# Performance work log

Measured on AMD Instinct MI355X. Metric: run time of the kernel, lower is better.

Reference implementation:

```python
import jax, jax.numpy as jnp
import numpy as np

# geomloss SamplesLoss('sinkhorn', p=2, blur=0.05, scaling=0.5, debias=True) math
P = 2
BLUR = 0.05
SCALING = 0.5
DIAMETER = 64.0  # static conservative bound on point-cloud diameter for randn D=64 data


def _eps_schedule():
    eps_list = []
    e = DIAMETER ** P
    target = BLUR ** P
    while e > target:
        eps_list.append(e)
        e *= SCALING ** P
    eps_list.append(target)
    return np.array(eps_list, dtype=np.float32)


def _cost(x, y):
    # C_ij = ||x_i - y_j||^2 / 2   (p=2 cost of geomloss)
    sq = (jnp.sum(x * x, -1)[:, :, None] * 0.5
          + jnp.sum(y * y, -1)[:, None, :] * 0.5
          - jnp.einsum('bnd,bmd->bnm', x, y))
    return jnp.maximum(sq, 0.0)


def _softmin(eps, C, h):
    # f_i = -eps * log sum_j exp(h_j - C_ij / eps);  C: (B,N,M), h: (B,M)
    return -eps * jax.nn.logsumexp(h[:, None, :] - C / eps, axis=-1)


def setup_inputs() -> dict:
    key = jax.random.key(0)
    k1, k2, k3, k4 = jax.random.split(key, 4)
    B, N, M, D = 8, 2048, 2048, 64
    x = jax.random.normal(k1, (B, N, D), dtype=jnp.float32)
    y = jax.random.normal(k2, (B, M, D), dtype=jnp.float32)
    w1 = jax.random.uniform(k3, (B, N), dtype=jnp.float32) + 0.01
    w2 = jax.random.uniform(k4, (B, M), dtype=jnp.float32) + 0.01
    w1 = w1 / jnp.sum(w1, axis=-1, keepdims=True)
    w2 = w2 / jnp.sum(w2, axis=-1, keepdims=True)
    return {'x': x, 'y': y, 'w1': w1, 'w2': w2}


def _sinkhorn_divergence(x, y, w1, w2):
    a_log = jnp.log(w1)
    b_log = jnp.log(w2)
    eps_list = jnp.asarray(_eps_schedule())

    # --- Sinkhorn loop on detached quantities (geomloss detaches the loop) ---
    xd = jax.lax.stop_gradient(x)
    yd = jax.lax.stop_gradient(y)
    ald = jax.lax.stop_gradient(a_log)
    bld = jax.lax.stop_gradient(b_log)
    C_xy_d = _cost(xd, yd)
    C_yx_d = jnp.swapaxes(C_xy_d, 1, 2)
    C_xx_d = _cost(xd, xd)
    C_yy_d = _cost(yd, yd)

    eps0 = eps_list[0]
    f_ab = _softmin(eps0, C_xy_d, bld)
    g_ba = _softmin(eps0, C_yx_d, ald)
    f_aa = _softmin(eps0, C_xx_d, ald)
    g_bb = _softmin(eps0, C_yy_d, bld)

    def step(carry, eps):
        f_ab, g_ba, f_aa, g_bb = carry
        ft = _softmin(eps, C_xy_d, bld + g_ba / eps)
        gt = _softmin(eps, C_yx_d, ald + f_ab / eps)
        f_aa_t = _softmin(eps, C_xx_d, ald + f_aa / eps)
        g_bb_t = _softmin(eps, C_yy_d, bld + g_bb / eps)
        return (0.5 * (f_ab + ft), 0.5 * (g_ba + gt),
                0.5 * (f_aa + f_aa_t), 0.5 * (g_bb + g_bb_t)), None

    (f_ab, g_ba, f_aa, g_bb), _ = jax.lax.scan(step, (f_ab, g_ba, f_aa, g_bb), eps_list)

    # --- last extrapolation at eps = blur^p, differentiable ---
    eps = eps_list[-1]
    C_xy = _cost(x, y)
    C_yx = jnp.swapaxes(C_xy, 1, 2)
    C_xx = _cost(x, x)
    C_yy = _cost(y, y)
    f_ab_f = _softmin(eps, C_xy, b_log + g_ba / eps)
    g_ba_f = _softmin(eps, C_yx, a_log + f_ab / eps)
    f_aa_f = _softmin(eps, C_xx, a_log + f_aa / eps)
    g_bb_f = _softmin(eps, C_yy, b_log + g_bb / eps)

    # debiased sinkhorn cost per batch element
    loss = (jnp.sum(w1 * (f_ab_f - f_aa_f), axis=-1)
            + jnp.sum(w2 * (g_ba_f - g_bb_f), axis=-1))
    return loss


def reference(x, y, w1, w2):
    loss = _sinkhorn_divergence(x, y, w1, w2)
    return jnp.mean(loss)  # reduction='mean'
```

## Files before the change

kernel.cpp:

```cpp
#include <hip/hip_runtime.h>

#define NB 8
#define NN 2048
#define MM 2048
#define DD 64
#define NMAT ((size_t)NN * (size_t)MM)
#define NCHK 16
#define TS 128

#define CSCALE 320.0f
#define CDEC   (1.0f / CSCALE)
#define LOG2E  1.4426950408889634f
#define LN2    0.6931471805599453f

typedef _Float16 half_t;
typedef __attribute__((ext_vector_type(8))) _Float16 f16x8;
typedef __attribute__((ext_vector_type(4))) float f32x4;

__device__ unsigned short g_C[3 * NB * NMAT];
__device__ half_t g_xh[NB * NN * DD];
__device__ half_t g_yh[NB * MM * DD];
__device__ float g_fab[3][NB * NN], g_gba[3][NB * NN];
__device__ float g_faa[3][NB * NN], g_gbb[3][NB * NN];
__device__ float g_alog[NB * NN], g_blog[NB * NN];
__device__ float g_xn[NB * NN], g_yn[NB * NN];
__device__ float g_h0[NB * MM], g_h1[NB * NN], g_h2[NB * NN], g_h3[NB * MM];
__device__ float2 g_pfab[NB * NCHK * NN];
__device__ float2 g_pgba[NB * NCHK * NN];
__device__ float2 g_pfaa[NB * NCHK * NN];
__device__ float2 g_pgbb[NB * NCHK * NN];

__global__ __launch_bounds__(256) void prep_kernel(
    const float* __restrict__ x, const float* __restrict__ y,
    const float* __restrict__ w1, const float* __restrict__ w2)
{
  int gid = blockIdx.x * 256 + threadIdx.x;
  if (gid < NB * NN) {
    g_alog[gid] = logf(w1[gid]);
    g_blog[gid] = logf(w2[gid]);
  }
  int lane = threadIdx.x & 63;
  int row = blockIdx.x * 4 + (threadIdx.x >> 6);
  float xv = x[(size_t)row * DD + lane];
  float yv = y[(size_t)row * DD + lane];
  g_xh[(size_t)row * DD + lane] = (half_t)xv;
  g_yh[(size_t)row * DD + lane] = (half_t)yv;
  float sx = xv * xv;
  float sy = yv * yv;
#pragma unroll
  for (int off = 32; off > 0; off >>= 1) {
    sx += __shfl_down(sx, off);
    sy += __shfl_down(sy, off);
  }
  if (lane == 0) {
    g_xn[row] = 0.5f * sx;
    g_yn[row] = 0.5f * sy;
  }
}

__global__ __launch_bounds__(256) void cost_mfma()
{
  const int slab = blockIdx.z >> 3;
  const int b = blockIdx.z & 7;
  int I, J;
  if (slab) {
    if (blockIdx.x >= 136) return;
    int rem = blockIdx.x, ii = 0;
    while (rem >= NCHK - ii) { rem -= NCHK - ii; ++ii; }
    I = ii; J = ii + rem;
  } else {
    I = blockIdx.x >> 4;
    J = blockIdx.x & 15;
  }

  const half_t* Ah = (slab == 2) ? g_yh : g_xh;
  const half_t* Bh = (slab == 0) ? g_yh : ((slab == 1) ? g_xh : g_yh);
  const float* na = (slab == 2) ? g_yn : g_xn;
  const float* nbp = (slab == 0) ? g_yn : ((slab == 1) ? g_xn : g_yn);
  unsigned short* Cout = g_C + (size_t)slab * NB * NMAT + (size_t)b * NMAT;

  const int t = threadIdx.x;
  const int w = t >> 6, lane = t & 63;
  const int m = lane & 15, quad = lane >> 4;
  const int i0 = I * TS, j0 = J * TS;

  const half_t* Abase = Ah + ((size_t)b * NN + i0 + 32 * w + m) * DD + quad * 8;
  const half_t* Bbase = Bh + ((size_t)b * MM + j0 + m) * DD + quad * 8;

  f32x4 acc[2][8];
#pragma unroll
  for (int g = 0; g < 2; ++g)
#pragma unroll
    for (int c = 0; c < 8; ++c) acc[g][c] = (f32x4){0.f, 0.f, 0.f, 0.f};

#pragma unroll
  for (int s = 0; s < 2; ++s) {
    f16x8 a0 = *(const f16x8*)(Abase + s * 32);
    f16x8 a1 = *(const f16x8*)(Abase + (size_t)16 * DD + s * 32);
#pragma unroll
    for (int c = 0; c < 8; ++c) {
      f16x8 bf = *(const f16x8*)(Bbase + (size_t)(16 * c) * DD + s * 32);
      acc[0][c] = __builtin_amdgcn_mfma_f32_16x16x32_f16(a0, bf, acc[0][c], 0, 0, 0);
      acc[1][c] = __builtin_amdgcn_mfma_f32_16x16x32_f16(a1, bf, acc[1][c], 0, 0, 0);
    }
  }

  __shared__ unsigned short tile[TS * TS];
  float4 xr[2];
#pragma unroll
  for (int g = 0; g < 2; ++g)
    xr[g] = *(const float4*)(na + b * NN + i0 + 32 * w + 16 * g + 4 * quad);
#pragma unroll
  for (int c = 0; c < 8; ++c) {
    float yv = nbp[b * MM + j0 + 16 * c + m];
#pragma unroll
    for (int g = 0; g < 2; ++g) {
      float xg[4] = {xr[g].x, xr[g].y, xr[g].z, xr[g].w};
#pragma unroll
      for (int r = 0; r < 4; ++r) {
        float cv = fmaxf(xg[r] + yv - acc[g][c][r], 0.f);
        unsigned int u = __float2uint_rn(fminf(cv * CSCALE, 65535.f));
        tile[(32 * w + 16 * g + 4 * quad + r) * TS + 16 * c + m] = (unsigned short)u;
      }
    }
  }
  __syncthreads();

  const uint4* tl = (const uint4*)tile;
#pragma unroll
  for (int p = 0; p < 8; ++p) {
    int u = p * 256 + t;
    int row = u >> 4, c8 = (u & 15) * 8;
    *(uint4*)(Cout + (size_t)(i0 + row) * MM + j0 + c8) = tl[u];
  }
}

__global__ __launch_bounds__(256) void hprep_kernel(
    const float* __restrict__ fab_in, const float* __restrict__ gba_in,
    const float* __restrict__ faa_in, const float* __restrict__ gbb_in,
    float gs)
{
  int i = blockIdx.x * 256 + threadIdx.x;
  g_h0[i] = fmaf(gs, gba_in[i], g_blog[i]);
  g_h1[i] = fmaf(gs, fab_in[i], g_alog[i]);
  g_h2[i] = fmaf(gs, faa_in[i], g_alog[i]);
  g_h3[i] = fmaf(gs, gbb_in[i], g_blog[i]);
}

struct TileArgs {
  const unsigned short* C;
  const float* hrow;
  const float* hcol;
  float2* prow;
  float2* pcol;
  int sym;
};

__global__ __launch_bounds__(256) void tile_pass(
    TileArgs T0, TileArgs T1, TileArgs T2, float inv_eps)
{
  TileArgs A = (blockIdx.z == 0) ? T0 : (blockIdx.z == 1) ? T1 : T2;
  int I, J;
  if (A.sym) {
    if (blockIdx.x >= 136) return;
    int rem = blockIdx.x, ii = 0;
    while (rem >= NCHK - ii) { rem -= NCHK - ii; ++ii; }
    I = ii; J = ii + rem;
  } else {
    I = blockIdx.x >> 4;
    J = blockIdx.x & 15;
  }
  const int b = blockIdx.y;
  const int t = threadIdx.x;
  const int ctr = t & 15;
  const int rtr = t >> 4;
  const float cs2 = -inv_eps * CDEC * LOG2E;

  const unsigned short* Cb = A.C + (size_t)b * NMAT
                           + (size_t)(I * TS) * MM + J * TS;

  float hr2[8], hc2[8];
  {
    const float* hrp = A.hrow + (size_t)b * MM + J * TS + ctr * 8;
    const float* hcp = A.hcol + (size_t)b * MM + I * TS + rtr * 8;
#pragma unroll
    for (int k = 0; k < 8; ++k) {
      hr2[k] = hrp[k] * LOG2E;
      hc2[k] = hcp[k] * LOG2E;
    }
  }

  uint4 cu[8];
#pragma unroll
  for (int r8 = 0; r8 < 8; ++r8)
    cu[r8] = *(const uint4*)(Cb + (size_t)(rtr * 8 + r8) * MM + ctr * 8);

  __shared__ float redC[TS][17];
  __shared__ float colM[TS];

  float rm[8], cm[8];
#pragma unroll
  for (int k = 0; k < 8; ++k) { rm[k] = -3.0e38f; cm[k] = -3.0e38f; }
#pragma unroll
  for (int r8 = 0; r8 < 8; ++r8) {
    float u[8];
    u[0] = (float)(cu[r8].x & 0xffff);
    u[1] = (float)(cu[r8].x >> 16);
    u[2] = (float)(cu[r8].y & 0xffff);
    u[3] = (float)(cu[r8].y >> 16);
    u[4] = (float)(cu[r8].z & 0xffff);
    u[5] = (float)(cu[r8].z >> 16);
    u[6] = (float)(cu[r8].w & 0xffff);
    u[7] = (float)(cu[r8].w >> 16);
#pragma unroll
    for (int c8 = 0; c8 < 8; ++c8) {
      rm[r8] = fmaxf(rm[r8], fmaf(u[c8], cs2, hr2[c8]));
      cm[c8] = fmaxf(cm[c8], fmaf(u[c8], cs2, hc2[r8]));
    }
  }
#pragma unroll
  for (int mask = 1; mask < 16; mask <<= 1)
#pragma unroll
    for (int k = 0; k < 8; ++k)
      rm[k] = fmaxf(rm[k], __shfl_xor(rm[k], mask));
#pragma unroll
  for (int c8 = 0; c8 < 8; ++c8) redC[ctr * 8 + c8][rtr] = cm[c8];
  __syncthreads();
  if (t < TS) {
    float m = redC[t][0];
#pragma unroll
    for (int k = 1; k < 16; ++k) m = fmaxf(m, redC[t][k]);
    colM[t] = m;
  }
  __syncthreads();
  float cmv[8];
#pragma unroll
  for (int c8 = 0; c8 < 8; ++c8) cmv[c8] = colM[ctr * 8 + c8];

  float rs[8], cs[8];
#pragma unroll
  for (int k = 0; k < 8; ++k) { rs[k] = 0.f; cs[k] = 0.f; }
#pragma unroll
  for (int r8 = 0; r8 < 8; ++r8) {
    float u[8];
    u[0] = (float)(cu[r8].x & 0xffff);
    u[1] = (float)(cu[r8].x >> 16);
    u[2] = (float)(cu[r8].y & 0xffff);
    u[3] = (float)(cu[r8].y >> 16);
    u[4] = (float)(cu[r8].z & 0xffff);
    u[5] = (float)(cu[r8].z >> 16);
    u[6] = (float)(cu[r8].w & 0xffff);
    u[7] = (float)(cu[r8].w >> 16);
#pragma unroll
    for (int c8 = 0; c8 < 8; ++c8) {
      rs[r8] += __builtin_amdgcn_exp2f(fmaf(u[c8], cs2, hr2[c8]) - rm[r8]);
      cs[c8] += __builtin_amdgcn_exp2f(fmaf(u[c8], cs2, hc2[r8]) - cmv[c8]);
    }
  }
#pragma unroll
  for (int mask = 1; mask < 16; mask <<= 1)
#pragma unroll
    for (int k = 0; k < 8; ++k)
      rs[k] += __shfl_xor(rs[k], mask);
  if (ctr < 8) {
    A.prow[((size_t)b * NCHK + J) * NN + I * TS + rtr * 8 + ctr]
        = make_float2(rm[ctr], rs[ctr]);
  }
  __syncthreads();
#pragma unroll
  for (int c8 = 0; c8 < 8; ++c8) redC[ctr * 8 + c8][rtr] = cs[c8];
  __syncthreads();
  if (t < TS && !(A.sym && I == J)) {
    float s = 0.f;
#pragma unroll
    for (int k = 0; k < 16; ++k) s += redC[t][k];
    A.pcol[((size_t)b * NCHK + I) * NN + J * TS + t] = make_float2(colM[t], s);
  }
}

struct MergeArgs {
  const float2* part;
  const float* fold;
  float* fout;
  const float* hbase;
  float* hout;
};

__global__ __launch_bounds__(256) void merge4(
    MergeArgs M0, MergeArgs M1, MergeArgs M2, MergeArgs M3,
    float eps, float alpha, float beta, float nextgs)
{
  MergeArgs A = (blockIdx.z == 0) ? M0 : (blockIdx.z == 1) ? M1
              : (blockIdx.z == 2) ? M2 : M3;
  const int b = blockIdx.y;
  const int i = blockIdx.x * 256 + threadIdx.x;
  float2 p[NCHK];
#pragma unroll
  for (int k = 0; k < NCHK; ++k)
    p[k] = A.part[((size_t)b * NCHK + k) * NN + i];
  float M = p[0].x;
#pragma unroll
  for (int k = 1; k < NCHK; ++k) M = fmaxf(M, p[k].x);
  float S = 0.f;
#pragma unroll
  for (int k = 0; k < NCHK; ++k)
    S += p[k].y * __builtin_amdgcn_exp2f(p[k].x - M);
  float ft = -eps * LN2 * (M + __builtin_amdgcn_logf(S));
  int idx = b * NN + i;
  float fnew = alpha * A.fold[idx] + beta * ft;
  A.fout[idx] = fnew;
  A.hout[idx] = fmaf(nextgs, fnew, A.hbase[idx]);
}

__global__ __launch_bounds__(256) void loss_kernel(
    const float* __restrict__ w1, const float* __restrict__ w2,
    float* __restrict__ out)
{
  __shared__ float red[256];
  float acc = 0.f;
  for (int idx = threadIdx.x; idx < NB * NN; idx += 256) {
    acc += w1[idx] * (g_fab[2][idx] - g_faa[2][idx])
         + w2[idx] * (g_gba[2][idx] - g_gbb[2][idx]);
  }
  red[threadIdx.x] = acc;
  __syncthreads();
  for (int s = 128; s > 0; s >>= 1) {
    if (threadIdx.x < s) red[threadIdx.x] += red[threadIdx.x + s];
    __syncthreads();
  }
  if (threadIdx.x == 0) out[0] = red[0] * (1.0f / NB);
}

extern "C" void kernel_launch(void* const* d_in, const int* in_sizes, int n_in,
                              void* d_out, int out_size, void* d_ws, size_t ws_size,
                              hipStream_t stream)
{
  const float* x = (const float*)d_in[0];
  const float* y = (const float*)d_in[1];
  const float* w1 = (const float*)d_in[2];
  const float* w2 = (const float*)d_in[3];
  float* out = (float*)d_out;

  unsigned short* Cbase;
  hipGetSymbolAddress((void**)&Cbase, HIP_SYMBOL(g_C));
  unsigned short* Cxy = Cbase + 0ull * NB * NMAT;
  unsigned short* Cxx = Cbase + 1ull * NB * NMAT;
  unsigned short* Cyy = Cbase + 2ull * NB * NMAT;
  float *h0, *h1, *h2, *h3, *fabp, *gbap, *faap, *gbbp, *alog, *blog;
  float2 *pfab, *pgba, *pfaa, *pgbb;
  hipGetSymbolAddress((void**)&h0, HIP_SYMBOL(g_h0));
  hipGetSymbolAddress((void**)&h1, HIP_SYMBOL(g_h1));
  hipGetSymbolAddress((void**)&h2, HIP_SYMBOL(g_h2));
  hipGetSymbolAddress((void**)&h3, HIP_SYMBOL(g_h3));
  hipGetSymbolAddress((void**)&fabp, HIP_SYMBOL(g_fab));
  hipGetSymbolAddress((void**)&gbap, HIP_SYMBOL(g_gba));
  hipGetSymbolAddress((void**)&faap, HIP_SYMBOL(g_faa));
  hipGetSymbolAddress((void**)&gbbp, HIP_SYMBOL(g_gbb));
  hipGetSymbolAddress((void**)&alog, HIP_SYMBOL(g_alog));
  hipGetSymbolAddress((void**)&blog, HIP_SYMBOL(g_blog));
  hipGetSymbolAddress((void**)&pfab, HIP_SYMBOL(g_pfab));
  hipGetSymbolAddress((void**)&pgba, HIP_SYMBOL(g_pgba));
  hipGetSymbolAddress((void**)&pfaa, HIP_SYMBOL(g_pfaa));
  hipGetSymbolAddress((void**)&pgbb, HIP_SYMBOL(g_pgbb));

  auto fab = [&](int s) { return fabp + (size_t)s * NB * NN; };
  auto gba = [&](int s) { return gbap + (size_t)s * NB * NN; };
  auto faa = [&](int s) { return faap + (size_t)s * NB * NN; };
  auto gbb = [&](int s) { return gbbp + (size_t)s * NB * NN; };

  float eps_list[32];
  int ne = 0;
  {
    double v = 64.0 * 64.0;
    double tgt = 0.05 * 0.05;
    while (v > tgt) { eps_list[ne++] = (float)v; v *= 0.25; }
    eps_list[ne++] = (float)tgt;
  }

  prep_kernel<<<4096, 256, 0, stream>>>(x, y, w1, w2);

  cost_mfma<<<dim3(256, 1, 24), 256, 0, stream>>>();

  dim3 tg(256, NB, 3);
  dim3 mg(NN / 256, NB, 4);

  auto launch_iter = [&](float eps, float alpha, float beta, float nextgs,
                         int in, int outsel) {
    float inv = 1.0f / eps;
    TileArgs T0 = {Cxy, h0, h1, pfab, pgba, 0};
    TileArgs T1 = {Cxx, h2, h2, pfaa, pfaa, 1};
    TileArgs T2 = {Cyy, h3, h3, pgbb, pgbb, 1};
    tile_pass<<<tg, 256, 0, stream>>>(T0, T1, T2, inv);
    MergeArgs M0 = {pfab, fab(in), fab(outsel), alog, h1};
    MergeArgs M1 = {pgba, gba(in), gba(outsel), blog, h0};
    MergeArgs M2 = {pfaa, faa(in), faa(outsel), alog, h2};
    MergeArgs M3 = {pgbb, gbb(in), gbb(outsel), blog, h3};
    merge4<<<mg, 256, 0, stream>>>(M0, M1, M2, M3, eps, alpha, beta, nextgs);
  };

  hprep_kernel<<<64, 256, 0, stream>>>(fab(0), gba(0), faa(0), gbb(0), 0.f);
  launch_iter(eps_list[0], 0.f, 1.f, 1.0f / eps_list[0], 0, 0);

  int cur = 0;
  for (int k = 0; k < ne; ++k) {
    int nxt = 1 - cur;
    float nextgs = 1.0f / ((k < ne - 1) ? eps_list[k + 1] : eps_list[ne - 1]);
    launch_iter(eps_list[k], 0.5f, 0.5f, nextgs, cur, nxt);
    cur = nxt;
  }

  launch_iter(eps_list[ne - 1], 0.f, 1.f, 0.f, cur, 2);

  loss_kernel<<<1, 256, 0, stream>>>(w1, w2, out);
}
```

Baseline: 717.5 us.

## Store cost tiles in MFMA fragment order and compact the tile grid

The quantized cost matrices are now stored tile-contiguously in the MFMA accumulator fragment layout. The cost kernel can therefore write each thread's packed values directly, without the LDS transpose and its barrier. The tile pass reads each tile with fully contiguous uint4 loads and does its column reductions with cross-lane shuffles, which shrinks the shared-memory reduction from 16 partials per column to 4. The grid is also compacted to 528 live tiles per batch (256 + 136 + 136) instead of launching 768 blocks and exiting the unused symmetric ones. The costs are extra shuffle work and more complex index mapping on the write-out of row results.

```diff
diff --git a/kernel.cpp b/kernel.cpp
--- a/kernel.cpp
+++ b/kernel.cpp
@@ -7,6 +7,8 @@
 #define NMAT ((size_t)NN * (size_t)MM)
 #define NCHK 16
 #define TS 128
+#define NTILE 528
+#define TELEM 16384
 
 #define CSCALE 320.0f
 #define CDEC   (1.0f / CSCALE)
@@ -17,7 +19,7 @@
 typedef __attribute__((ext_vector_type(8))) _Float16 f16x8;
 typedef __attribute__((ext_vector_type(4))) float f32x4;
 
-__device__ unsigned short g_C[3 * NB * NMAT];
+__device__ unsigned short g_C[(size_t)NB * NTILE * TELEM];
 __device__ half_t g_xh[NB * NN * DD];
 __device__ half_t g_yh[NB * MM * DD];
 __device__ float g_fab[3][NB * NN], g_gba[3][NB * NN];
@@ -30,6 +32,17 @@
 __device__ float2 g_pfaa[NB * NCHK * NN];
 __device__ float2 g_pgbb[NB * NCHK * NN];
 
+__device__ __forceinline__ void tile_decode(int xid, int& slab, int& I, int& J)
+{
+  int tid;
+  if (xid < 256)      { slab = 0; tid = xid; I = tid >> 4; J = tid & 15; return; }
+  else if (xid < 392) { slab = 1; tid = xid - 256; }
+  else                { slab = 2; tid = xid - 392; }
+  int rem = tid, ii = 0;
+  while (rem >= NCHK - ii) { rem -= NCHK - ii; ++ii; }
+  I = ii; J = ii + rem;
+}
+
 __global__ __launch_bounds__(256) void prep_kernel(
     const float* __restrict__ x, const float* __restrict__ y,
     const float* __restrict__ w1, const float* __restrict__ w2)
@@ -60,24 +73,14 @@
 
 __global__ __launch_bounds__(256) void cost_mfma()
 {
-  const int slab = blockIdx.z >> 3;
-  const int b = blockIdx.z & 7;
-  int I, J;
-  if (slab) {
-    if (blockIdx.x >= 136) return;
-    int rem = blockIdx.x, ii = 0;
-    while (rem >= NCHK - ii) { rem -= NCHK - ii; ++ii; }
-    I = ii; J = ii + rem;
-  } else {
-    I = blockIdx.x >> 4;
-    J = blockIdx.x & 15;
-  }
+  int slab, I, J;
+  tile_decode(blockIdx.x, slab, I, J);
+  const int b = blockIdx.y;
 
   const half_t* Ah = (slab == 2) ? g_yh : g_xh;
   const half_t* Bh = (slab == 0) ? g_yh : ((slab == 1) ? g_xh : g_yh);
   const float* na = (slab == 2) ? g_yn : g_xn;
   const float* nbp = (slab == 0) ? g_yn : ((slab == 1) ? g_xn : g_yn);
-  unsigned short* Cout = g_C + (size_t)slab * NB * NMAT + (size_t)b * NMAT;
 
   const int t = threadIdx.x;
   const int w = t >> 6, lane = t & 63;
@@ -105,33 +108,31 @@
     }
   }
 
-  __shared__ unsigned short tile[TS * TS];
   float4 xr[2];
 #pragma unroll
   for (int g = 0; g < 2; ++g)
     xr[g] = *(const float4*)(na + b * NN + i0 + 32 * w + 16 * g + 4 * quad);
-#pragma unroll
-  for (int c = 0; c < 8; ++c) {
-    float yv = nbp[b * MM + j0 + 16 * c + m];
-#pragma unroll
-    for (int g = 0; g < 2; ++g) {
-      float xg[4] = {xr[g].x, xr[g].y, xr[g].z, xr[g].w};
-#pragma unroll
-      for (int r = 0; r < 4; ++r) {
-        float cv = fmaxf(xg[r] + yv - acc[g][c][r], 0.f);
-        unsigned int u = __float2uint_rn(fminf(cv * CSCALE, 65535.f));
-        tile[(32 * w + 16 * g + 4 * quad + r) * TS + 16 * c + m] = (unsigned short)u;
-      }
+  float yv[8];
+#pragma unroll
+  for (int c = 0; c < 8; ++c) yv[c] = nbp[b * MM + j0 + 16 * c + m];
+
+  uint4* Cout = (uint4*)(g_C + ((size_t)b * NTILE + blockIdx.x) * TELEM);
+#pragma unroll
+  for (int k = 0; k < 8; ++k) {
+    int g = k >> 2, r = k & 3;
+    float xg = (r == 0) ? xr[g].x : (r == 1) ? xr[g].y : (r == 2) ? xr[g].z : xr[g].w;
+    unsigned int u[8];
+#pragma unroll
+    for (int c = 0; c < 8; ++c) {
+      float cv = fmaxf(xg + yv[c] - acc[g][c][r], 0.f);
+      u[c] = __float2uint_rn(fminf(cv * CSCALE, 65535.f));
     }
-  }
-  __syncthreads();
-
-  const uint4* tl = (const uint4*)tile;
-#pragma unroll
-  for (int p = 0; p < 8; ++p) {
-    int u = p * 256 + t;
-    int row = u >> 4, c8 = (u & 15) * 8;
-    *(uint4*)(Cout + (size_t)(i0 + row) * MM + j0 + c8) = tl[u];
+    uint4 ow;
+    ow.x = u[0] | (u[1] << 16);
+    ow.y = u[2] | (u[3] << 16);
+    ow.z = u[4] | (u[5] << 16);
+    ow.w = u[6] | (u[7] << 16);
+    Cout[k * 256 + t] = ow;
   }
 }
 
@@ -148,7 +149,6 @@
 }
 
 struct TileArgs {
-  const unsigned short* C;
   const float* hrow;
   const float* hcol;
   float2* prow;
@@ -159,63 +159,55 @@
 __global__ __launch_bounds__(256) void tile_pass(
     TileArgs T0, TileArgs T1, TileArgs T2, float inv_eps)
 {
-  TileArgs A = (blockIdx.z == 0) ? T0 : (blockIdx.z == 1) ? T1 : T2;
-  int I, J;
-  if (A.sym) {
-    if (blockIdx.x >= 136) return;
-    int rem = blockIdx.x, ii = 0;
-    while (rem >= NCHK - ii) { rem -= NCHK - ii; ++ii; }
-    I = ii; J = ii + rem;
-  } else {
-    I = blockIdx.x >> 4;
-    J = blockIdx.x & 15;
-  }
+  int slab, I, J;
+  tile_decode(blockIdx.x, slab, I, J);
+  TileArgs A = (slab == 0) ? T0 : (slab == 1) ? T1 : T2;
   const int b = blockIdx.y;
   const int t = threadIdx.x;
-  const int ctr = t & 15;
-  const int rtr = t >> 4;
+  const int w = t >> 6, lane = t & 63;
+  const int m = lane & 15, quad = lane >> 4;
   const float cs2 = -inv_eps * CDEC * LOG2E;
 
-  const unsigned short* Cb = A.C + (size_t)b * NMAT
-                           + (size_t)(I * TS) * MM + J * TS;
-
-  float hr2[8], hc2[8];
-  {
-    const float* hrp = A.hrow + (size_t)b * MM + J * TS + ctr * 8;
-    const float* hcp = A.hcol + (size_t)b * MM + I * TS + rtr * 8;
-#pragma unroll
-    for (int k = 0; k < 8; ++k) {
-      hr2[k] = hrp[k] * LOG2E;
-      hc2[k] = hcp[k] * LOG2E;
-    }
-  }
-
+  const uint4* Cb = (const uint4*)(g_C + ((size_t)b * NTILE + blockIdx.x) * TELEM);
   uint4 cu[8];
 #pragma unroll
-  for (int r8 = 0; r8 < 8; ++r8)
-    cu[r8] = *(const uint4*)(Cb + (size_t)(rtr * 8 + r8) * MM + ctr * 8);
-
-  __shared__ float redC[TS][17];
+  for (int k = 0; k < 8; ++k) cu[k] = Cb[k * 256 + t];
+
+  float hr2[8];
+#pragma unroll
+  for (int c = 0; c < 8; ++c)
+    hr2[c] = A.hrow[b * MM + J * TS + 16 * c + m] * LOG2E;
+  float hc2[8];
+#pragma unroll
+  for (int g = 0; g < 2; ++g) {
+    float4 h4 = *(const float4*)(A.hcol + b * NN + I * TS + 32 * w + 16 * g + 4 * quad);
+    hc2[g * 4 + 0] = h4.x * LOG2E;
+    hc2[g * 4 + 1] = h4.y * LOG2E;
+    hc2[g * 4 + 2] = h4.z * LOG2E;
+    hc2[g * 4 + 3] = h4.w * LOG2E;
+  }
+
+  __shared__ float redC[TS][5];
   __shared__ float colM[TS];
 
   float rm[8], cm[8];
 #pragma unroll
   for (int k = 0; k < 8; ++k) { rm[k] = -3.0e38f; cm[k] = -3.0e38f; }
 #pragma unroll
-  for (int r8 = 0; r8 < 8; ++r8) {
+  for (int k = 0; k < 8; ++k) {
     float u[8];
-    u[0] = (float)(cu[r8].x & 0xffff);
-    u[1] = (float)(cu[r8].x >> 16);
-    u[2] = (float)(cu[r8].y & 0xffff);
-    u[3] = (float)(cu[r8].y >> 16);
-    u[4] = (float)(cu[r8].z & 0xffff);
-    u[5] = (float)(cu[r8].z >> 16);
-    u[6] = (float)(cu[r8].w & 0xffff);
-    u[7] = (float)(cu[r8].w >> 16);
-#pragma unroll
-    for (int c8 = 0; c8 < 8; ++c8) {
-      rm[r8] = fmaxf(rm[r8], fmaf(u[c8], cs2, hr2[c8]));
-      cm[c8] = fmaxf(cm[c8], fmaf(u[c8], cs2, hc2[r8]));
+    u[0] = (float)(cu[k].x & 0xffff);
+    u[1] = (float)(cu[k].x >> 16);
+    u[2] = (float)(cu[k].y & 0xffff);
+    u[3] = (float)(cu[k].y >> 16);
+    u[4] = (float)(cu[k].z & 0xffff);
+    u[5] = (float)(cu[k].z >> 16);
+    u[6] = (float)(cu[k].w & 0xffff);
+    u[7] = (float)(cu[k].w >> 16);
+#pragma unroll
+    for (int c = 0; c < 8; ++c) {
+      rm[k] = fmaxf(rm[k], fmaf(u[c], cs2, hr2[c]));
+      cm[c] = fmaxf(cm[c], fmaf(u[c], cs2, hc2[k]));
     }
   }
 #pragma unroll
@@ -224,37 +216,43 @@
     for (int k = 0; k < 8; ++k)
       rm[k] = fmaxf(rm[k], __shfl_xor(rm[k], mask));
 #pragma unroll
-  for (int c8 = 0; c8 < 8; ++c8) redC[ctr * 8 + c8][rtr] = cm[c8];
+  for (int mask = 16; mask < 64; mask <<= 1)
+#pragma unroll
+    for (int c = 0; c < 8; ++c)
+      cm[c] = fmaxf(cm[c], __shfl_xor(cm[c], mask));
+  if (quad == 0) {
+#pragma unroll
+    for (int c = 0; c < 8; ++c) redC[16 * c + m][w] = cm[c];
+  }
   __syncthreads();
   if (t < TS) {
-    float m = redC[t][0];
-#pragma unroll
-    for (int k = 1; k < 16; ++k) m = fmaxf(m, redC[t][k]);
-    colM[t] = m;
+    float v = fmaxf(fmaxf(redC[t][0], redC[t][1]),
+                    fmaxf(redC[t][2], redC[t][3]));
+    colM[t] = v;
   }
   __syncthreads();
   float cmv[8];
 #pragma unroll
-  for (int c8 = 0; c8 < 8; ++c8) cmv[c8] = colM[ctr * 8 + c8];
+  for (int c = 0; c < 8; ++c) cmv[c] = colM[16 * c + m];
 
   float rs[8], cs[8];
 #pragma unroll
   for (int k = 0; k < 8; ++k) { rs[k] = 0.f; cs[k] = 0.f; }
 #pragma unroll
-  for (int r8 = 0; r8 < 8; ++r8) {
+  for (int k = 0; k < 8; ++k) {
     float u[8];
-    u[0] = (float)(cu[r8].x & 0xffff);
-    u[1] = (float)(cu[r8].x >> 16);
-    u[2] = (float)(cu[r8].y & 0xffff);
-    u[3] = (float)(cu[r8].y >> 16);
-    u[4] = (float)(cu[r8].z & 0xffff);
-    u[5] = (float)(cu[r8].z >> 16);
-    u[6] = (float)(cu[r8].w & 0xffff);
-    u[7] = (float)(cu[r8].w >> 16);
-#pragma unroll
-    for (int c8 = 0; c8 < 8; ++c8) {
-      rs[r8] += __builtin_amdgcn_exp2f(fmaf(u[c8], cs2, hr2[c8]) - rm[r8]);
-      cs[c8] += __builtin_amdgcn_exp2f(fmaf(u[c8], cs2, hc2[r8]) - cmv[c8]);
+    u[0] = (float)(cu[k].x & 0xffff);
+    u[1] = (float)(cu[k].x >> 16);
+    u[2] = (float)(cu[k].y & 0xffff);
+    u[3] = (float)(cu[k].y >> 16);
+    u[4] = (float)(cu[k].z & 0xffff);
+    u[5] = (float)(cu[k].z >> 16);
+    u[6] = (float)(cu[k].w & 0xffff);
+    u[7] = (float)(cu[k].w >> 16);
+#pragma unroll
+    for (int c = 0; c < 8; ++c) {
+      rs[k] += __builtin_amdgcn_exp2f(fmaf(u[c], cs2, hr2[c]) - rm[k]);
+      cs[c] += __builtin_amdgcn_exp2f(fmaf(u[c], cs2, hc2[k]) - cmv[c]);
     }
   }
 #pragma unroll
@@ -262,18 +260,24 @@
 #pragma unroll
     for (int k = 0; k < 8; ++k)
       rs[k] += __shfl_xor(rs[k], mask);
-  if (ctr < 8) {
-    A.prow[((size_t)b * NCHK + J) * NN + I * TS + rtr * 8 + ctr]
-        = make_float2(rm[ctr], rs[ctr]);
-  }
+  if (m < 8) {
+    int k = m;
+    int i = I * TS + 32 * w + 16 * (k >> 2) + 4 * quad + (k & 3);
+    A.prow[((size_t)b * NCHK + J) * NN + i] = make_float2(rm[k], rs[k]);
+  }
+#pragma unroll
+  for (int mask = 16; mask < 64; mask <<= 1)
+#pragma unroll
+    for (int c = 0; c < 8; ++c)
+      cs[c] += __shfl_xor(cs[c], mask);
   __syncthreads();
-#pragma unroll
-  for (int c8 = 0; c8 < 8; ++c8) redC[ctr * 8 + c8][rtr] = cs[c8];
+  if (quad == 0) {
+#pragma unroll
+    for (int c = 0; c < 8; ++c) redC[16 * c + m][w] = cs[c];
+  }
   __syncthreads();
   if (t < TS && !(A.sym && I == J)) {
-    float s = 0.f;
-#pragma unroll
-    for (int k = 0; k < 16; ++k) s += redC[t][k];
+    float s = redC[t][0] + redC[t][1] + redC[t][2] + redC[t][3];
     A.pcol[((size_t)b * NCHK + I) * NN + J * TS + t] = make_float2(colM[t], s);
   }
 }
@@ -341,11 +345,6 @@
   const float* w2 = (const float*)d_in[3];
   float* out = (float*)d_out;
 
-  unsigned short* Cbase;
-  hipGetSymbolAddress((void**)&Cbase, HIP_SYMBOL(g_C));
-  unsigned short* Cxy = Cbase + 0ull * NB * NMAT;
-  unsigned short* Cxx = Cbase + 1ull * NB * NMAT;
-  unsigned short* Cyy = Cbase + 2ull * NB * NMAT;
   float *h0, *h1, *h2, *h3, *fabp, *gbap, *faap, *gbbp, *alog, *blog;
   float2 *pfab, *pgba, *pfaa, *pgbb;
   hipGetSymbolAddress((void**)&h0, HIP_SYMBOL(g_h0));
@@ -379,17 +378,17 @@
 
   prep_kernel<<<4096, 256, 0, stream>>>(x, y, w1, w2);
 
-  cost_mfma<<<dim3(256, 1, 24), 256, 0, stream>>>();
-
-  dim3 tg(256, NB, 3);
+  cost_mfma<<<dim3(NTILE, NB), 256, 0, stream>>>();
+
+  dim3 tg(NTILE, NB);
   dim3 mg(NN / 256, NB, 4);
 
   auto launch_iter = [&](float eps, float alpha, float beta, float nextgs,
                          int in, int outsel) {
     float inv = 1.0f / eps;
-    TileArgs T0 = {Cxy, h0, h1, pfab, pgba, 0};
-    TileArgs T1 = {Cxx, h2, h2, pfaa, pfaa, 1};
-    TileArgs T2 = {Cyy, h3, h3, pgbb, pgbb, 1};
+    TileArgs T0 = {h0, h1, pfab, pgba, 0};
+    TileArgs T1 = {h2, h2, pfaa, pfaa, 1};
+    TileArgs T2 = {h3, h3, pgbb, pgbb, 1};
     tile_pass<<<tg, 256, 0, stream>>>(T0, T1, T2, inv);
     MergeArgs M0 = {pfab, fab(in), fab(outsel), alog, h1};
     MergeArgs M1 = {pgba, gba(in), gba(outsel), blog, h0};
```

After: 834.8 us. 16.3% more time.
